# Performance work log

Measured on AMD Instinct MI355X. Metric: run time of the kernel, lower is better.

## Reference

```python
import jax, jax.numpy as jnp
import numpy as np

N_NODES = 100000


def _gcn_layer(x, src, dst, nrm, W, b):
    # x: [N, Din] -> [N, Dout]. GCNConv: linear transform then deg-normalized scatter-add.
    h = x @ W                                  # [N, Dout]
    msg = h[src] * nrm[:, None]               # gather + per-edge normalization, [E', Dout]
    agg = jax.ops.segment_sum(msg, dst, num_segments=N_NODES)
    return agg + b


def setup_inputs() -> dict:
    key = jax.random.key(0)
    ks = jax.random.split(key, 16)
    x = jax.random.normal(ks[0], (N_NODES, 128), dtype=jnp.float32)
    edge_index = jax.random.randint(ks[1], (2, 1600000), 0, N_NODES, dtype=jnp.int64)
    d = {"x": x, "edge_index": edge_index}
    dims = [(128, 64), (64, 64), (64, 64), (64, 64), (64, 64), (64, 64)]
    for i, (din, dout) in enumerate(dims):
        scale = 1.0 / np.sqrt(din)
        d[f"W{i+1}"] = jax.random.uniform(ks[2 + 2 * i], (din, dout), jnp.float32, -scale, scale)
        d[f"b{i+1}"] = jnp.zeros((dout,), jnp.float32)
    return d


def reference(x, edge_index, W1, b1, W2, b2, W3, b3, W4, b4, W5, b5, W6, b6):
    # Add self-loops (GCNConv default), symmetric normalization D^-1/2 A D^-1/2.
    loops = jnp.arange(N_NODES, dtype=edge_index.dtype)
    src = jnp.concatenate([edge_index[0], loops])
    dst = jnp.concatenate([edge_index[1], loops])
    deg = jax.ops.segment_sum(jnp.ones_like(dst, dtype=x.dtype), dst, num_segments=N_NODES)
    dinv = jnp.where(deg > 0, jax.lax.rsqrt(deg), 0.0)
    nrm = dinv[src] * dinv[dst]               # per-edge norm coefficient, [E']

    h = x
    for (W, b) in ((W1, b1), (W2, b2), (W3, b3), (W4, b4), (W5, b5), (W6, b6)):
        h = jax.nn.relu(_gcn_layer(h, src, dst, nrm, W, b))
        # eval mode: dropout is identity
    return jax.nn.log_softmax(h, axis=-1)
```

## Files before the change

### kernel.cpp

```cpp
#include <hip/hip_runtime.h>
#include <hip/hip_fp16.h>
#include <math.h>

#define N_NODES 100000
#define N_EDGES 1600000
#define NB 1563
#define CAP 2048
#define NBLK_S 128
#define CHUNK (N_EDGES / NBLK_S)

typedef _Float16 half8_t __attribute__((ext_vector_type(8)));
typedef float floatx4 __attribute__((ext_vector_type(4)));


__global__ __launch_bounds__(256) void k_hist(const int* __restrict__ dst,
                                              int* __restrict__ ghist) {
    __shared__ int hist[NB];
    int blk = blockIdx.x, t = threadIdx.x;
    for (int i = t; i < NB; i += 256) hist[i] = 0;
    __syncthreads();
    const int4* dq = (const int4*)(dst + blk * CHUNK);
    const int nq = CHUNK >> 2;
    for (int i = t; i < nq; i += 256) {
        int4 d = dq[i];
        atomicAdd(&hist[d.x >> 6], 1);
        atomicAdd(&hist[d.y >> 6], 1);
        atomicAdd(&hist[d.z >> 6], 1);
        atomicAdd(&hist[d.w >> 6], 1);
    }
    __syncthreads();
    for (int i = t; i < NB; i += 256) ghist[i * NBLK_S + blk] = hist[i];
}

__global__ void k_scanb(int* __restrict__ ghist, int* __restrict__ btot) {
    __shared__ int s[NBLK_S];
    int b = blockIdx.x, t = threadIdx.x;
    int v = ghist[b * NBLK_S + t];
    s[t] = v;
    __syncthreads();
    for (int off = 1; off < NBLK_S; off <<= 1) {
        int a = (t >= off) ? s[t - off] : 0;
        __syncthreads();
        s[t] += a;
        __syncthreads();
    }
    ghist[b * NBLK_S + t] = s[t] - v;
    if (t == NBLK_S - 1) btot[b] = s[t];
}

__global__ void k_scant(const int* __restrict__ btot, int* __restrict__ bbase,
                        int* __restrict__ rowptr) {
    __shared__ int s[1024];
    __shared__ int carry;
    int t = threadIdx.x;
    if (t == 0) carry = 0;
    __syncthreads();
    for (int chunk = 0; chunk < 2; ++chunk) {
        int i = chunk * 1024 + t;
        int v = (i < NB) ? btot[i] : 0;
        s[t] = v;
        __syncthreads();
        for (int off = 1; off < 1024; off <<= 1) {
            int a = (t >= off) ? s[t - off] : 0;
            __syncthreads();
            s[t] += a;
            __syncthreads();
        }
        if (i < NB) bbase[i] = carry + s[t] - v;
        int total = carry + s[1023];
        __syncthreads();
        if (t == 0) carry = total;
        __syncthreads();
    }
    if (t == 0) rowptr[N_NODES] = N_EDGES;
}

__global__ __launch_bounds__(256) void k_scatter(const int* __restrict__ src,
                                                 const int* __restrict__ dst,
                                                 const int* __restrict__ ghist,
                                                 const int* __restrict__ bbase,
                                                 unsigned* __restrict__ bentry) {
    __shared__ int cursor[NB];
    int blk = blockIdx.x, t = threadIdx.x;
    for (int i = t; i < NB; i += 256)
        cursor[i] = bbase[i] + ghist[i * NBLK_S + blk];
    __syncthreads();
    const int4* dq = (const int4*)(dst + blk * CHUNK);
    const int4* sq = (const int4*)(src + blk * CHUNK);
    const int nq = CHUNK >> 2;
    for (int i = t; i < nq; i += 256) {
        int4 d = dq[i];
        int4 s = sq[i];
        int p0 = atomicAdd(&cursor[d.x >> 6], 1);
        int p1 = atomicAdd(&cursor[d.y >> 6], 1);
        int p2 = atomicAdd(&cursor[d.z >> 6], 1);
        int p3 = atomicAdd(&cursor[d.w >> 6], 1);
        bentry[p0] = ((unsigned)(d.x & 63) << 17) | (unsigned)s.x;
        bentry[p1] = ((unsigned)(d.y & 63) << 17) | (unsigned)s.y;
        bentry[p2] = ((unsigned)(d.z & 63) << 17) | (unsigned)s.z;
        bentry[p3] = ((unsigned)(d.w & 63) << 17) | (unsigned)s.w;
    }
}

__global__ __launch_bounds__(256) void k_fill2(const int* __restrict__ btot,
                                               const int* __restrict__ bbase,
                                               const unsigned* __restrict__ bentry,
                                               int* __restrict__ rowptr,
                                               float* __restrict__ dinv,
                                               int* __restrict__ colv) {
    __shared__ unsigned ent[CAP];
    __shared__ int hist[64];
    __shared__ int cursor[64];
    int b = blockIdx.x;
    int t = threadIdx.x;
    int cnt = btot[b]; if (cnt > CAP) cnt = CAP;
    int base = bbase[b];
    if (t < 64) hist[t] = 0;
    __syncthreads();
    const unsigned* be = bentry + base;
    for (int i = t; i < cnt; i += 256) {
        unsigned e = be[i];
        ent[i] = e;
        atomicAdd(&hist[e >> 17], 1);
    }
    __syncthreads();
    if (t < 64) {
        int v = hist[t];
        int incl = v;
#pragma unroll
        for (int off = 1; off < 64; off <<= 1) {
            int a = __shfl_up(incl, off);
            if (t >= off) incl += a;
        }
        int excl = incl - v;
        cursor[t] = excl;
        int node = (b << 6) + t;
        if (node < N_NODES) {
            rowptr[node] = base + excl;
            dinv[node] = rsqrtf((float)(v + 1));
        }
    }
    __syncthreads();
    for (int i = t; i < cnt; i += 256) {
        unsigned e = ent[i];
        int pos = base + atomicAdd(&cursor[e >> 17], 1);
        colv[pos] = (int)(e & 0x1FFFF);
    }
}


__global__ void k_prepw(const float* __restrict__ W1, const float* __restrict__ W2,
                        const float* __restrict__ W3, const float* __restrict__ W4,
                        const float* __restrict__ W5, const float* __restrict__ W6,
                        __half* __restrict__ wt) {
    int l = blockIdx.x;
    const float* W = (l == 0) ? W1 : (l == 1) ? W2 : (l == 2) ? W3
                   : (l == 3) ? W4 : (l == 4) ? W5 : W6;
    int din = (l == 0) ? 128 : 64;
    __half* dstp = wt + ((l == 0) ? 0 : 8192 + (l - 1) * 4096);
    int n = 64 * din;
    for (int i = threadIdx.x; i < n; i += blockDim.x) {
        int col = i / din, k = i - col * din;
        dstp[i] = __float2half(W[k * 64 + col]);
    }
}


__global__ void k_xhalf(const float* __restrict__ x, __half* __restrict__ xh, int n4) {
    int i = blockIdx.x * blockDim.x + threadIdx.x;
    if (i < n4) {
        float4 v = ((const float4*)x)[i];
        union { uint2 u; __half2 h2[2]; } pk;
        pk.h2[0] = __floats2half2_rn(v.x, v.y);
        pk.h2[1] = __floats2half2_rn(v.z, v.w);
        ((uint2*)xh)[i] = pk.u;
    }
}


template<int DIN>
__global__ __launch_bounds__(256) void k_gemm(const __half* __restrict__ in,
                                              const __half* __restrict__ Wt,
                                              const float* __restrict__ dinv,
                                              __half* __restrict__ h) {
    int tid  = threadIdx.x;
    int lane = tid & 63;
    int node0 = blockIdx.x * 64 + (tid >> 6) * 16;
    if (node0 >= N_NODES) return;
    int lr = lane & 15;
    int lk = (lane >> 4) * 8;

    int arow = node0 + lr; if (arow >= N_NODES) arow = N_NODES - 1;
    const __half* ap = in + (size_t)arow * DIN + lk;
    const __half* bp = Wt + (size_t)lr * DIN + lk;

    floatx4 acc0 = {0.f, 0.f, 0.f, 0.f}, acc1 = acc0, acc2 = acc0, acc3 = acc0;
#pragma unroll
    for (int kc = 0; kc < DIN / 32; ++kc) {
        half8_t a  = *(const half8_t*)(ap + kc * 32);
        half8_t b0 = *(const half8_t*)(bp + kc * 32);
        half8_t b1 = *(const half8_t*)(bp + kc * 32 + 16 * DIN);
        half8_t b2 = *(const half8_t*)(bp + kc * 32 + 32 * DIN);
        half8_t b3 = *(const half8_t*)(bp + kc * 32 + 48 * DIN);
        acc0 = __builtin_amdgcn_mfma_f32_16x16x32_f16(a, b0, acc0, 0, 0, 0);
        acc1 = __builtin_amdgcn_mfma_f32_16x16x32_f16(a, b1, acc1, 0, 0, 0);
        acc2 = __builtin_amdgcn_mfma_f32_16x16x32_f16(a, b2, acc2, 0, 0, 0);
        acc3 = __builtin_amdgcn_mfma_f32_16x16x32_f16(a, b3, acc3, 0, 0, 0);
    }

    int rbase = node0 + (lane >> 4) * 4;
#pragma unroll
    for (int r = 0; r < 4; ++r) {
        int row = rbase + r;
        if (row < N_NODES) {
            float dn = dinv[row];
            __half* op = h + ((size_t)row << 6) + lr;
            op[0]  = __float2half(acc0[r] * dn);
            op[16] = __float2half(acc1[r] * dn);
            op[32] = __float2half(acc2[r] * dn);
            op[48] = __float2half(acc3[r] * dn);
        }
    }
}


template<int LAST>
__global__ __launch_bounds__(256) void k_aggregate(const int* __restrict__ rowptr,
                                                   const int* __restrict__ colv,
                                                   const __half* __restrict__ h,
                                                   const float* __restrict__ dinv,
                                                   const float* __restrict__ bias,
                                                   __half* __restrict__ acta,
                                                   float* __restrict__ outf) {
    int tid  = threadIdx.x;
    int node = blockIdx.x * 16 + (tid >> 4);
    if (node >= N_NODES) return;
    int ql = tid & 15;

    int beg = rowptr[node], end = rowptr[node + 1];
    const __half* hp = h + (ql << 2);

    __half2 a0 = __floats2half2_rn(0.f, 0.f), a1 = a0, b0 = a0, b1 = a0;
    int k = beg;
    for (; k + 4 <= end; k += 4) {
        int s0 = colv[k], s1 = colv[k + 1], s2 = colv[k + 2], s3 = colv[k + 3];
        union { uint2 u; __half2 h2[2]; } v0, v1, v2, v3;
        v0.u = *(const uint2*)(hp + ((size_t)s0 << 6));
        v1.u = *(const uint2*)(hp + ((size_t)s1 << 6));
        v2.u = *(const uint2*)(hp + ((size_t)s2 << 6));
        v3.u = *(const uint2*)(hp + ((size_t)s3 << 6));
        a0 = __hadd2(a0, v0.h2[0]); a1 = __hadd2(a1, v0.h2[1]);
        b0 = __hadd2(b0, v1.h2[0]); b1 = __hadd2(b1, v1.h2[1]);
        a0 = __hadd2(a0, v2.h2[0]); a1 = __hadd2(a1, v2.h2[1]);
        b0 = __hadd2(b0, v3.h2[0]); b1 = __hadd2(b1, v3.h2[1]);
    }
    for (; k < end; ++k) {
        int s0 = colv[k];
        union { uint2 u; __half2 h2[2]; } v0;
        v0.u = *(const uint2*)(hp + ((size_t)s0 << 6));
        a0 = __hadd2(a0, v0.h2[0]); a1 = __hadd2(a1, v0.h2[1]);
    }
    a0 = __hadd2(a0, b0); a1 = __hadd2(a1, b1);

    float2 f0 = __half22float2(a0), f1 = __half22float2(a1);
    union { uint2 u; __half2 h2[2]; } sv;
    sv.u = *(const uint2*)(hp + ((size_t)node << 6));
    float2 s0f = __half22float2(sv.h2[0]), s1f = __half22float2(sv.h2[1]);
    float dn = dinv[node];
    float4 bv = ((const float4*)bias)[ql];
    float r0 = fmaxf(fmaf(f0.x + s0f.x, dn, bv.x), 0.f);
    float r1 = fmaxf(fmaf(f0.y + s0f.y, dn, bv.y), 0.f);
    float r2 = fmaxf(fmaf(f1.x + s1f.x, dn, bv.z), 0.f);
    float r3 = fmaxf(fmaf(f1.y + s1f.y, dn, bv.w), 0.f);

    if (LAST) {
        float m = fmaxf(fmaxf(r0, r1), fmaxf(r2, r3));
#pragma unroll
        for (int off = 1; off <= 8; off <<= 1) m = fmaxf(m, __shfl_xor(m, off));
        float ss = expf(r0 - m) + expf(r1 - m) + expf(r2 - m) + expf(r3 - m);
#pragma unroll
        for (int off = 1; off <= 8; off <<= 1) ss += __shfl_xor(ss, off);
        float lse = m + logf(ss);
        *(float4*)(outf + ((size_t)node << 6) + (ql << 2)) =
            make_float4(r0 - lse, r1 - lse, r2 - lse, r3 - lse);
    } else {
        union { uint2 u; __half2 h2[2]; } pk;
        pk.h2[0] = __floats2half2_rn(r0, r1);
        pk.h2[1] = __floats2half2_rn(r2, r3);
        *(uint2*)(acta + ((size_t)node << 6) + (ql << 2)) = pk.u;
    }
}


extern "C" void kernel_launch(void* const* d_in, const int* in_sizes, int n_in,
                              void* d_out, int out_size, void* d_ws, size_t ws_size,
                              hipStream_t stream) {
    const float* x = (const float*)d_in[0];
    const int* ei  = (const int*)d_in[1];
    const int* src = ei;
    const int* dst = ei + N_EDGES;

    const float* W[6];
    const float* b[6];
    for (int i = 0; i < 6; ++i) {
        W[i] = (const float*)d_in[2 + 2 * i];
        b[i] = (const float*)d_in[3 + 2 * i];
    }
    float* out = (float*)d_out;

    char* p = (char*)d_ws;
    __half* h      = (__half*)p; p += (size_t)N_NODES * 64 * 2;
    __half* act    = (__half*)p; p += (size_t)N_NODES * 64 * 2;
    __half* xh     = (__half*)p; p += (size_t)N_NODES * 128 * 2;
    __half* wt     = (__half*)p; p += 28672 * 2;
    int*    rowptr = (int*)p;    p += (size_t)(N_NODES + 1) * 4;
    float*  dinv   = (float*)p;  p += (size_t)N_NODES * 4;
    int*    colv   = (int*)p;
    unsigned* bentry = (unsigned*)h;
    int*    ghist = (int*)(bentry + (size_t)N_EDGES);
    int*    btot  = ghist + (size_t)NB * NBLK_S;
    int*    bbase = btot + NB;

    const int nb_q    = (N_NODES + 15) / 16;
    const int nb_tile = (N_NODES + 63) / 64;
    const int n4      = N_NODES * 128 / 4;

    k_prepw<<<6, 256, 0, stream>>>(W[0], W[1], W[2], W[3], W[4], W[5], wt);
    k_xhalf<<<(n4 + 255) / 256, 256, 0, stream>>>(x, xh, n4);

    k_hist<<<NBLK_S, 256, 0, stream>>>(dst, ghist);
    k_scanb<<<NB, NBLK_S, 0, stream>>>(ghist, btot);
    k_scant<<<1, 1024, 0, stream>>>(btot, bbase, rowptr);
    k_scatter<<<NBLK_S, 256, 0, stream>>>(src, dst, ghist, bbase, bentry);
    k_fill2<<<NB, 256, 0, stream>>>(btot, bbase, bentry, rowptr, dinv, colv);

    for (int l = 0; l < 6; ++l) {
        if (l == 0)
            k_gemm<128><<<nb_tile, 256, 0, stream>>>(xh, wt, dinv, h);
        else
            k_gemm<64><<<nb_tile, 256, 0, stream>>>(act, wt + 8192 + (l - 1) * 4096, dinv, h);
        if (l == 5)
            k_aggregate<1><<<nb_q, 256, 0, stream>>>(rowptr, colv, h, dinv, b[l], act, out);
        else
            k_aggregate<0><<<nb_q, 256, 0, stream>>>(rowptr, colv, h, dinv, b[l], act, out);
    }
}
```

Before: 381.9 us.

## Fuse fp32-to-fp16 input conversion into first GEMM, widen sort blocks, unroll aggregation

Removes the separate x-to-half conversion kernel and its buffer; the first-layer GEMM now reads fp32 rows and converts in registers. The histogram and scatter kernels for the CSR build move from 256 to 1024 threads per block. The aggregation gather loop is unrolled to 8 neighbours with four independent half2 accumulator pairs to expose more memory-level parallelism. Trade-offs: the first GEMM reads twice the bytes per A fragment, and larger blocks may change LDS atomic contention.

```diff
diff --git a/kernel.cpp b/kernel.cpp
--- a/kernel.cpp
+++ b/kernel.cpp
@@ -13,15 +13,15 @@
 typedef float floatx4 __attribute__((ext_vector_type(4)));
 
 
-__global__ __launch_bounds__(256) void k_hist(const int* __restrict__ dst,
-                                              int* __restrict__ ghist) {
+__global__ __launch_bounds__(1024) void k_hist(const int* __restrict__ dst,
+                                               int* __restrict__ ghist) {
     __shared__ int hist[NB];
     int blk = blockIdx.x, t = threadIdx.x;
-    for (int i = t; i < NB; i += 256) hist[i] = 0;
+    for (int i = t; i < NB; i += 1024) hist[i] = 0;
     __syncthreads();
     const int4* dq = (const int4*)(dst + blk * CHUNK);
     const int nq = CHUNK >> 2;
-    for (int i = t; i < nq; i += 256) {
+    for (int i = t; i < nq; i += 1024) {
         int4 d = dq[i];
         atomicAdd(&hist[d.x >> 6], 1);
         atomicAdd(&hist[d.y >> 6], 1);
@@ -29,7 +29,7 @@
         atomicAdd(&hist[d.w >> 6], 1);
     }
     __syncthreads();
-    for (int i = t; i < NB; i += 256) ghist[i * NBLK_S + blk] = hist[i];
+    for (int i = t; i < NB; i += 1024) ghist[i * NBLK_S + blk] = hist[i];
 }
 
 __global__ void k_scanb(int* __restrict__ ghist, int* __restrict__ btot) {
@@ -75,20 +75,20 @@
     if (t == 0) rowptr[N_NODES] = N_EDGES;
 }
 
-__global__ __launch_bounds__(256) void k_scatter(const int* __restrict__ src,
-                                                 const int* __restrict__ dst,
-                                                 const int* __restrict__ ghist,
-                                                 const int* __restrict__ bbase,
-                                                 unsigned* __restrict__ bentry) {
+__global__ __launch_bounds__(1024) void k_scatter(const int* __restrict__ src,
+                                                  const int* __restrict__ dst,
+                                                  const int* __restrict__ ghist,
+                                                  const int* __restrict__ bbase,
+                                                  unsigned* __restrict__ bentry) {
     __shared__ int cursor[NB];
     int blk = blockIdx.x, t = threadIdx.x;
-    for (int i = t; i < NB; i += 256)
+    for (int i = t; i < NB; i += 1024)
         cursor[i] = bbase[i] + ghist[i * NBLK_S + blk];
     __syncthreads();
     const int4* dq = (const int4*)(dst + blk * CHUNK);
     const int4* sq = (const int4*)(src + blk * CHUNK);
     const int nq = CHUNK >> 2;
-    for (int i = t; i < nq; i += 256) {
+    for (int i = t; i < nq; i += 1024) {
         int4 d = dq[i];
         int4 s = sq[i];
         int p0 = atomicAdd(&cursor[d.x >> 6], 1);
@@ -166,20 +166,8 @@
 }
 
 
-__global__ void k_xhalf(const float* __restrict__ x, __half* __restrict__ xh, int n4) {
-    int i = blockIdx.x * blockDim.x + threadIdx.x;
-    if (i < n4) {
-        float4 v = ((const float4*)x)[i];
-        union { uint2 u; __half2 h2[2]; } pk;
-        pk.h2[0] = __floats2half2_rn(v.x, v.y);
-        pk.h2[1] = __floats2half2_rn(v.z, v.w);
-        ((uint2*)xh)[i] = pk.u;
-    }
-}
-
-
-template<int DIN>
-__global__ __launch_bounds__(256) void k_gemm(const __half* __restrict__ in,
+template<int DIN, int F32IN>
+__global__ __launch_bounds__(256) void k_gemm(const void* __restrict__ in,
                                               const __half* __restrict__ Wt,
                                               const float* __restrict__ dinv,
                                               __half* __restrict__ h) {
@@ -191,13 +179,24 @@
     int lk = (lane >> 4) * 8;
 
     int arow = node0 + lr; if (arow >= N_NODES) arow = N_NODES - 1;
-    const __half* ap = in + (size_t)arow * DIN + lk;
+    const __half* ap  = (const __half*)in + (size_t)arow * DIN + lk;
+    const float*  ap32 = (const float*)in + (size_t)arow * DIN + lk;
     const __half* bp = Wt + (size_t)lr * DIN + lk;
 
     floatx4 acc0 = {0.f, 0.f, 0.f, 0.f}, acc1 = acc0, acc2 = acc0, acc3 = acc0;
 #pragma unroll
     for (int kc = 0; kc < DIN / 32; ++kc) {
-        half8_t a  = *(const half8_t*)(ap + kc * 32);
+        half8_t a;
+        if (F32IN) {
+            float4 f0 = *(const float4*)(ap32 + kc * 32);
+            float4 f1 = *(const float4*)(ap32 + kc * 32 + 4);
+            a[0] = (_Float16)f0.x; a[1] = (_Float16)f0.y;
+            a[2] = (_Float16)f0.z; a[3] = (_Float16)f0.w;
+            a[4] = (_Float16)f1.x; a[5] = (_Float16)f1.y;
+            a[6] = (_Float16)f1.z; a[7] = (_Float16)f1.w;
+        } else {
+            a = *(const half8_t*)(ap + kc * 32);
+        }
         half8_t b0 = *(const half8_t*)(bp + kc * 32);
         half8_t b1 = *(const half8_t*)(bp + kc * 32 + 16 * DIN);
         half8_t b2 = *(const half8_t*)(bp + kc * 32 + 32 * DIN);
@@ -240,30 +239,54 @@
     int beg = rowptr[node], end = rowptr[node + 1];
     const __half* hp = h + (ql << 2);
 
-    __half2 a0 = __floats2half2_rn(0.f, 0.f), a1 = a0, b0 = a0, b1 = a0;
+    __half2 z = __floats2half2_rn(0.f, 0.f);
+    __half2 A0 = z, A1 = z, B0 = z, B1 = z, C0 = z, C1 = z, D0 = z, D1 = z;
+    union UV { uint2 u; __half2 h2[2]; };
     int k = beg;
-    for (; k + 4 <= end; k += 4) {
-        int s0 = colv[k], s1 = colv[k + 1], s2 = colv[k + 2], s3 = colv[k + 3];
-        union { uint2 u; __half2 h2[2]; } v0, v1, v2, v3;
+    for (; k + 8 <= end; k += 8) {
+        int s0 = colv[k],     s1 = colv[k + 1], s2 = colv[k + 2], s3 = colv[k + 3];
+        int s4 = colv[k + 4], s5 = colv[k + 5], s6 = colv[k + 6], s7 = colv[k + 7];
+        UV v0, v1, v2, v3, v4, v5, v6, v7;
         v0.u = *(const uint2*)(hp + ((size_t)s0 << 6));
         v1.u = *(const uint2*)(hp + ((size_t)s1 << 6));
         v2.u = *(const uint2*)(hp + ((size_t)s2 << 6));
         v3.u = *(const uint2*)(hp + ((size_t)s3 << 6));
-        a0 = __hadd2(a0, v0.h2[0]); a1 = __hadd2(a1, v0.h2[1]);
-        b0 = __hadd2(b0, v1.h2[0]); b1 = __hadd2(b1, v1.h2[1]);
-        a0 = __hadd2(a0, v2.h2[0]); a1 = __hadd2(a1, v2.h2[1]);
-        b0 = __hadd2(b0, v3.h2[0]); b1 = __hadd2(b1, v3.h2[1]);
+        v4.u = *(const uint2*)(hp + ((size_t)s4 << 6));
+        v5.u = *(const uint2*)(hp + ((size_t)s5 << 6));
+        v6.u = *(const uint2*)(hp + ((size_t)s6 << 6));
+        v7.u = *(const uint2*)(hp + ((size_t)s7 << 6));
+        A0 = __hadd2(A0, v0.h2[0]); A1 = __hadd2(A1, v0.h2[1]);
+        B0 = __hadd2(B0, v1.h2[0]); B1 = __hadd2(B1, v1.h2[1]);
+        C0 = __hadd2(C0, v2.h2[0]); C1 = __hadd2(C1, v2.h2[1]);
+        D0 = __hadd2(D0, v3.h2[0]); D1 = __hadd2(D1, v3.h2[1]);
+        A0 = __hadd2(A0, v4.h2[0]); A1 = __hadd2(A1, v4.h2[1]);
+        B0 = __hadd2(B0, v5.h2[0]); B1 = __hadd2(B1, v5.h2[1]);
+        C0 = __hadd2(C0, v6.h2[0]); C1 = __hadd2(C1, v6.h2[1]);
+        D0 = __hadd2(D0, v7.h2[0]); D1 = __hadd2(D1, v7.h2[1]);
+    }
+    for (; k + 4 <= end; k += 4) {
+        int s0 = colv[k], s1 = colv[k + 1], s2 = colv[k + 2], s3 = colv[k + 3];
+        UV v0, v1, v2, v3;
+        v0.u = *(const uint2*)(hp + ((size_t)s0 << 6));
+        v1.u = *(const uint2*)(hp + ((size_t)s1 << 6));
+        v2.u = *(const uint2*)(hp + ((size_t)s2 << 6));
+        v3.u = *(const uint2*)(hp + ((size_t)s3 << 6));
+        A0 = __hadd2(A0, v0.h2[0]); A1 = __hadd2(A1, v0.h2[1]);
+        B0 = __hadd2(B0, v1.h2[0]); B1 = __hadd2(B1, v1.h2[1]);
+        C0 = __hadd2(C0, v2.h2[0]); C1 = __hadd2(C1, v2.h2[1]);
+        D0 = __hadd2(D0, v3.h2[0]); D1 = __hadd2(D1, v3.h2[1]);
     }
     for (; k < end; ++k) {
         int s0 = colv[k];
-        union { uint2 u; __half2 h2[2]; } v0;
+        UV v0;
         v0.u = *(const uint2*)(hp + ((size_t)s0 << 6));
-        a0 = __hadd2(a0, v0.h2[0]); a1 = __hadd2(a1, v0.h2[1]);
-    }
-    a0 = __hadd2(a0, b0); a1 = __hadd2(a1, b1);
-
-    float2 f0 = __half22float2(a0), f1 = __half22float2(a1);
-    union { uint2 u; __half2 h2[2]; } sv;
+        A0 = __hadd2(A0, v0.h2[0]); A1 = __hadd2(A1, v0.h2[1]);
+    }
+    A0 = __hadd2(__hadd2(A0, B0), __hadd2(C0, D0));
+    A1 = __hadd2(__hadd2(A1, B1), __hadd2(C1, D1));
+
+    float2 f0 = __half22float2(A0), f1 = __half22float2(A1);
+    UV sv;
     sv.u = *(const uint2*)(hp + ((size_t)node << 6));
     float2 s0f = __half22float2(sv.h2[0]), s1f = __half22float2(sv.h2[1]);
     float dn = dinv[node];
@@ -284,7 +307,7 @@
         *(float4*)(outf + ((size_t)node << 6) + (ql << 2)) =
             make_float4(r0 - lse, r1 - lse, r2 - lse, r3 - lse);
     } else {
-        union { uint2 u; __half2 h2[2]; } pk;
+        UV pk;
         pk.h2[0] = __floats2half2_rn(r0, r1);
         pk.h2[1] = __floats2half2_rn(r2, r3);
         *(uint2*)(acta + ((size_t)node << 6) + (ql << 2)) = pk.u;
@@ -311,7 +334,6 @@
     char* p = (char*)d_ws;
     __half* h      = (__half*)p; p += (size_t)N_NODES * 64 * 2;
     __half* act    = (__half*)p; p += (size_t)N_NODES * 64 * 2;
-    __half* xh     = (__half*)p; p += (size_t)N_NODES * 128 * 2;
     __half* wt     = (__half*)p; p += 28672 * 2;
     int*    rowptr = (int*)p;    p += (size_t)(N_NODES + 1) * 4;
     float*  dinv   = (float*)p;  p += (size_t)N_NODES * 4;
@@ -323,22 +345,20 @@
 
     const int nb_q    = (N_NODES + 15) / 16;
     const int nb_tile = (N_NODES + 63) / 64;
-    const int n4      = N_NODES * 128 / 4;
 
     k_prepw<<<6, 256, 0, stream>>>(W[0], W[1], W[2], W[3], W[4], W[5], wt);
-    k_xhalf<<<(n4 + 255) / 256, 256, 0, stream>>>(x, xh, n4);
-
-    k_hist<<<NBLK_S, 256, 0, stream>>>(dst, ghist);
+
+    k_hist<<<NBLK_S, 1024, 0, stream>>>(dst, ghist);
     k_scanb<<<NB, NBLK_S, 0, stream>>>(ghist, btot);
     k_scant<<<1, 1024, 0, stream>>>(btot, bbase, rowptr);
-    k_scatter<<<NBLK_S, 256, 0, stream>>>(src, dst, ghist, bbase, bentry);
+    k_scatter<<<NBLK_S, 1024, 0, stream>>>(src, dst, ghist, bbase, bentry);
     k_fill2<<<NB, 256, 0, stream>>>(btot, bbase, bentry, rowptr, dinv, colv);
 
     for (int l = 0; l < 6; ++l) {
         if (l == 0)
-            k_gemm<128><<<nb_tile, 256, 0, stream>>>(xh, wt, dinv, h);
+            k_gemm<128, 1><<<nb_tile, 256, 0, stream>>>(x, wt, dinv, h);
         else
-            k_gemm<64><<<nb_tile, 256, 0, stream>>>(act, wt + 8192 + (l - 1) * 4096, dinv, h);
+            k_gemm<64, 0><<<nb_tile, 256, 0, stream>>>(act, wt + 8192 + (l - 1) * 4096, dinv, h);
         if (l == 5)
             k_aggregate<1><<<nb_q, 256, 0, stream>>>(rowptr, colv, h, dinv, b[l], act, out);
         else
```

New measurement: 351.5 us. 1.09x faster.
